# Kernel optimization log

Hardware: AMD Instinct MI355X
Metric: run time of the kernel (lower is better)

The kernel has to match this reference:

```python
import jax, jax.numpy as jnp
import numpy as np

EMB = 1024
HEADS = 16

def setup_inputs() -> dict:
    key = jax.random.key(0)
    ks = jax.random.split(key, 9)
    s = 1.0 / np.sqrt(EMB)
    x = jax.random.normal(ks[0], (2, 2048, EMB), dtype=jnp.float32)
    Wq = jax.random.normal(ks[1], (EMB, EMB), dtype=jnp.float32) * s
    bq = jax.random.normal(ks[2], (EMB,), dtype=jnp.float32) * s
    Wk = jax.random.normal(ks[3], (EMB, EMB), dtype=jnp.float32) * s
    bk = jax.random.normal(ks[4], (EMB,), dtype=jnp.float32) * s
    Wv = jax.random.normal(ks[5], (EMB, EMB), dtype=jnp.float32) * s
    bv = jax.random.normal(ks[6], (EMB,), dtype=jnp.float32) * s
    Wo = jax.random.normal(ks[7], (EMB, EMB), dtype=jnp.float32) * s
    bo = jax.random.normal(ks[8], (EMB,), dtype=jnp.float32) * s
    return {"x": x, "Wq": Wq, "bq": bq, "Wk": Wk, "bk": bk, "Wv": Wv, "bv": bv, "Wo": Wo, "bo": bo}

def reference(x, Wq, bq, Wk, bk, Wv, bv, Wo, bo):
    B, N, E = x.shape
    H = HEADS
    D = E // H
    # q/k/v projections, split heads: b n (h d) -> b h n d
    def proj(W, b):
        y = jnp.einsum('bne,ef->bnf', x, W.T) + b
        return y.reshape(B, N, H, D).transpose(0, 2, 1, 3)
    q = proj(Wq, bq)
    k = proj(Wk, bk)
    v = proj(Wv, bv)
    energy = jnp.einsum('bhqd,bhkd->bhqk', q, k)
    scaling = jnp.asarray(E, x.dtype) ** 0.5  # note: sqrt(emb_size), as in source
    att = jax.nn.softmax(energy / scaling, axis=-1)
    out = jnp.einsum('bhqk,bhkd->bhqd', att, v)
    out = out.transpose(0, 2, 1, 3).reshape(B, N, E)  # b h n d -> b n (h d)
    return jnp.einsum('bne,ef->bnf', out, Wo.T) + bo
```

## Files before the change

### kernel.cpp

```cpp
#include <hip/hip_runtime.h>
#include <hip/hip_bf16.h>
#include <stdint.h>

typedef __bf16 bf16;
typedef __bf16 bf16x8 __attribute__((ext_vector_type(8)));
typedef __bf16 bf16x4 __attribute__((ext_vector_type(4)));
typedef __bf16 bf16x2 __attribute__((ext_vector_type(2)));
typedef float  f32x4  __attribute__((ext_vector_type(4)));
typedef float  f32x16 __attribute__((ext_vector_type(16)));
typedef unsigned int uint;

#define MFMA(a,b,c)   __builtin_amdgcn_mfma_f32_16x16x32_bf16((a),(b),(c),0,0,0)
#define MFMA32(a,b,c) __builtin_amdgcn_mfma_f32_32x32x16_bf16((a),(b),(c),0,0,0)
#define EXP2(x)       __builtin_amdgcn_exp2f(x)

__device__ __forceinline__ void gload_lds16(const void* g, void* lds) {
  __builtin_amdgcn_global_load_lds(
      (const __attribute__((address_space(1))) uint32_t*)g,
      (__attribute__((address_space(3))) uint32_t*)lds, 16, 0, 0);
}

__device__ __forceinline__ uint pk_bf16(float lo, float hi) {
  bf16x2 v; v[0] = (bf16)lo; v[1] = (bf16)hi;
  return __builtin_bit_cast(uint, v);
}

__global__ __launch_bounds__(256) void k_cvt(
    const float* __restrict__ x,
    const float* __restrict__ wq, const float* __restrict__ wk,
    const float* __restrict__ wv, const float* __restrict__ wo,
    bf16* __restrict__ xb, bf16* __restrict__ wqb, bf16* __restrict__ wkb,
    bf16* __restrict__ wvb, bf16* __restrict__ wob)
{
  int r = blockIdx.y;
  const float* s; bf16* d; int n;
  switch (r) {
    case 0: s = x;  d = xb;  n = 4194304; break;
    case 1: s = wq; d = wqb; n = 1048576; break;
    case 2: s = wk; d = wkb; n = 1048576; break;
    case 3: s = wv; d = wvb; n = 1048576; break;
    default: s = wo; d = wob; n = 1048576; break;
  }
  int i = (blockIdx.x * 256 + threadIdx.x) * 8;
  if (i >= n) return;
  const float4* sp = (const float4*)(s + i);
  float4 a = sp[0], b = sp[1];
  bf16x8 o;
  o[0]=(bf16)a.x; o[1]=(bf16)a.y; o[2]=(bf16)a.z; o[3]=(bf16)a.w;
  o[4]=(bf16)b.x; o[5]=(bf16)b.y; o[6]=(bf16)b.z; o[7]=(bf16)b.w;
  *(bf16x8*)(d + i) = o;
}

__global__ __launch_bounds__(256) void k_gemm_qkv(
    const bf16* __restrict__ A,
    const bf16* __restrict__ Wq, const bf16* __restrict__ Wk, const bf16* __restrict__ Wv,
    const float* __restrict__ bq, const float* __restrict__ bk, const float* __restrict__ bv,
    bf16* __restrict__ Qw, bf16* __restrict__ Kw, bf16* __restrict__ Vtw)
{
  __shared__ __align__(16) char As[8192];
  __shared__ __align__(16) char Bs[8192];
  int tid = threadIdx.x;
  int wv4 = tid >> 6, l = tid & 63, lo = l & 15, hi = l >> 4;
  int mt = blockIdx.x;
  int ft = blockIdx.y;
  int wsel = ft >> 3;
  const bf16* W = (wsel == 0) ? Wq : (wsel == 1) ? Wk : Wv;
  const float* bias = (wsel == 0) ? bq : (wsel == 1) ? bk : bv;
  int f0 = (ft & 7) * 128;
  const bf16* Ab = A + (size_t)mt * 128 * 1024;
  const bf16* Wb = W + (size_t)f0 * 1024;
  int wm = wv4 >> 1, wf = wv4 & 1;
  f32x4 acc[4][4];
  #pragma unroll
  for (int i = 0; i < 4; i++)
    #pragma unroll
    for (int j = 0; j < 4; j++) acc[i][j] = (f32x4){0.f, 0.f, 0.f, 0.f};

  for (int k0 = 0; k0 < 1024; k0 += 32) {
    __syncthreads();
    #pragma unroll
    for (int p = 0; p < 2; p++) {
      int e = p * 256 + tid;
      int row = e >> 2, sl = e & 3;
      gload_lds16(Ab + row * 1024 + k0 + sl * 8, As + (p * 256 + wv4 * 64) * 16);
      gload_lds16(Wb + row * 1024 + k0 + sl * 8, Bs + (p * 256 + wv4 * 64) * 16);
    }
    __syncthreads();
    bf16x8 af[4], bfr[4];
    #pragma unroll
    for (int ms = 0; ms < 4; ms++)
      af[ms] = *(const bf16x8*)(As + ((wm * 64 + ms * 16 + lo) * 32 + hi * 8) * 2);
    #pragma unroll
    for (int fs = 0; fs < 4; fs++)
      bfr[fs] = *(const bf16x8*)(Bs + ((wf * 64 + fs * 16 + lo) * 32 + hi * 8) * 2);
    #pragma unroll
    for (int ms = 0; ms < 4; ms++)
      #pragma unroll
      for (int fs = 0; fs < 4; fs++)
        acc[ms][fs] = MFMA(af[ms], bfr[fs], acc[ms][fs]);
  }

  float bv4[4];
  #pragma unroll
  for (int fs = 0; fs < 4; fs++) bv4[fs] = bias[f0 + wf * 64 + fs * 16 + lo];
  #pragma unroll
  for (int ms = 0; ms < 4; ms++) {
    #pragma unroll
    for (int fs = 0; fs < 4; fs++) {
      int fl = f0 + wf * 64 + fs * 16 + lo;
      int h = fl >> 6, dd = fl & 63;
      #pragma unroll
      for (int r = 0; r < 4; r++) {
        int m = mt * 128 + wm * 64 + ms * 16 + hi * 4 + r;
        int b = m >> 11, n = m & 2047;
        float val = acc[ms][fs][r] + bv4[fs];
        if (wsel == 0)      Qw[(((size_t)(b * 16 + h) * 2048 + n) * 64) + dd] = (bf16)(val * 0.0450842199527801f);
        else if (wsel == 1) Kw[(((size_t)(b * 16 + h) * 2048 + n) * 64) + dd] = (bf16)val;
        else                Vtw[(((size_t)(b * 16 + h) * 64 + dd) * 2048) + n] = (bf16)val;
      }
    }
  }
}

__global__ __launch_bounds__(256, 1) void k_attn(
    const bf16* __restrict__ Q, const bf16* __restrict__ K,
    const bf16* __restrict__ Vt, bf16* __restrict__ O)
{
  __shared__ __align__(16) char Ks[2][8192];
  __shared__ __align__(16) char Vs[2][8192];
  int tid = threadIdx.x;
  int wid = tid >> 6, l = tid & 63;
  int lq = l & 31, hi1 = l >> 5;
  int qt = blockIdx.x, bh = blockIdx.y;
  int q0 = qt * 256 + wid * 64;
  const bf16* Kb = K + (size_t)bh * 2048 * 64;
  const bf16* Vb = Vt + (size_t)bh * 64 * 2048;
  const bf16* Qb = Q + ((size_t)bh * 2048 + q0) * 64 + hi1 * 8;

  bf16x8 qf0[4], qf1[4];
  #pragma unroll
  for (int c = 0; c < 4; c++) {
    qf0[c] = *(const bf16x8*)(Qb + (size_t)lq * 64 + 16 * c);
    qf1[c] = *(const bf16x8*)(Qb + (size_t)(lq + 32) * 64 + 16 * c);
  }

  f32x16 o00, o01, o10, o11;
  f32x16 zz;
  #pragma unroll
  for (int r = 0; r < 16; r++) { zz[r] = 0.f; o00[r] = 0.f; o01[r] = 0.f; o10[r] = 0.f; o11[r] = 0.f; }
  float ls0 = 0.f, ls1 = 0.f;

  int srow = tid >> 3, slot = tid & 7;
  int swz = 16 * (slot ^ (srow & 7));
  int swk = lq & 7;
  uint4 k0r, k1r, v0r, v1r;
  #define STAGE(t) {                                                          \
    k0r = *(const uint4*)(Kb + (size_t)((t)*64 + srow) * 64 + slot * 8);      \
    k1r = *(const uint4*)(Kb + (size_t)((t)*64 + srow + 32) * 64 + slot * 8); \
    v0r = *(const uint4*)(Vb + (size_t)srow * 2048 + (t)*64 + slot * 8);      \
    v1r = *(const uint4*)(Vb + (size_t)(srow + 32) * 2048 + (t)*64 + slot * 8); }
  #define WRBUF(bi) {                                  \
    *(uint4*)(Ks[bi] + srow * 128 + swz)        = k0r; \
    *(uint4*)(Ks[bi] + (srow + 32) * 128 + swz) = k1r; \
    *(uint4*)(Vs[bi] + srow * 128 + swz)        = v0r; \
    *(uint4*)(Vs[bi] + (srow + 32) * 128 + swz) = v1r; }
  #define EXPSUM(S, T0, T1, T2, T3)                     \
    _Pragma("unroll")                                   \
    for (int r = 0; r < 16; r += 4) {                   \
      S[r]   = EXP2(S[r]);   T0 += S[r];                \
      S[r+1] = EXP2(S[r+1]); T1 += S[r+1];              \
      S[r+2] = EXP2(S[r+2]); T2 += S[r+2];              \
      S[r+3] = EXP2(S[r+3]); T3 += S[r+3];              \
    }
  #define PACK(dst, plo, phi)                                                \
    _Pragma("unroll")                                                        \
    for (int m = 0; m < 2; m++) {                                            \
      uint a0 = pk_bf16(plo[8*m+0], plo[8*m+1]);                             \
      uint b0 = pk_bf16(plo[8*m+4], plo[8*m+5]);                             \
      asm volatile("v_permlane32_swap_b32 %0, %1" : "+v"(a0), "+v"(b0));     \
      uint a1 = pk_bf16(plo[8*m+2], plo[8*m+3]);                             \
      uint b1 = pk_bf16(plo[8*m+6], plo[8*m+7]);                             \
      asm volatile("v_permlane32_swap_b32 %0, %1" : "+v"(a1), "+v"(b1));     \
      dst[m] = (uint4){a0, a1, b0, b1};                                      \
      uint c0 = pk_bf16(phi[8*m+0], phi[8*m+1]);                             \
      uint d0 = pk_bf16(phi[8*m+4], phi[8*m+5]);                             \
      asm volatile("v_permlane32_swap_b32 %0, %1" : "+v"(c0), "+v"(d0));     \
      uint c1 = pk_bf16(phi[8*m+2], phi[8*m+3]);                             \
      uint d1 = pk_bf16(phi[8*m+6], phi[8*m+7]);                             \
      asm volatile("v_permlane32_swap_b32 %0, %1" : "+v"(c1), "+v"(d1));     \
      dst[2+m] = (uint4){c0, c1, d0, d1};                                    \
    }

  STAGE(0);
  WRBUF(0);
  STAGE(1);

  for (int t = 0; t < 32; ++t) {
    __syncthreads();
    const char* Kc = Ks[t & 1];
    const char* Vc = Vs[t & 1];

    bf16x8 kf0[4], kf1[4];
    #pragma unroll
    for (int c = 0; c < 4; c++) {
      kf0[c] = *(const bf16x8*)(Kc + lq * 128 + 16 * ((2*c + hi1) ^ swk));
      kf1[c] = *(const bf16x8*)(Kc + (32 + lq) * 128 + 16 * ((2*c + hi1) ^ swk));
    }

    __builtin_amdgcn_s_setprio(1);
    f32x16 s00 = MFMA32(kf0[0], qf0[0], zz);
    f32x16 s01 = MFMA32(kf1[0], qf0[0], zz);
    f32x16 s10 = MFMA32(kf0[0], qf1[0], zz);
    f32x16 s11 = MFMA32(kf1[0], qf1[0], zz);
    #pragma unroll
    for (int c = 1; c < 4; c++) {
      s00 = MFMA32(kf0[c], qf0[c], s00);
      s01 = MFMA32(kf1[c], qf0[c], s01);
      s10 = MFMA32(kf0[c], qf1[c], s10);
      s11 = MFMA32(kf1[c], qf1[c], s11);
    }
    __builtin_amdgcn_s_setprio(0);

    float t0 = 0.f, t1 = 0.f, t2 = 0.f, t3 = 0.f;
    float u0 = 0.f, u1 = 0.f, u2 = 0.f, u3 = 0.f;
    EXPSUM(s00, t0, t1, t2, t3);
    EXPSUM(s01, t0, t1, t2, t3);
    EXPSUM(s10, u0, u1, u2, u3);
    EXPSUM(s11, u0, u1, u2, u3);
    ls0 += (t0 + t1) + (t2 + t3);
    ls1 += (u0 + u1) + (u2 + u3);

    uint4 pf0[4], pf1[4];
    PACK(pf0, s00, s01);
    PACK(pf1, s10, s11);

    __builtin_amdgcn_s_setprio(1);
    #pragma unroll
    for (int c = 0; c < 4; c++) {
      bf16x8 vf0 = *(const bf16x8*)(Vc + lq * 128 + 16 * ((2*c + hi1) ^ swk));
      bf16x8 vf1 = *(const bf16x8*)(Vc + (32 + lq) * 128 + 16 * ((2*c + hi1) ^ swk));
      bf16x8 p0b = __builtin_bit_cast(bf16x8, pf0[c]);
      bf16x8 p1b = __builtin_bit_cast(bf16x8, pf1[c]);
      o00 = MFMA32(vf0, p0b, o00);
      o01 = MFMA32(vf1, p0b, o01);
      o10 = MFMA32(vf0, p1b, o10);
      o11 = MFMA32(vf1, p1b, o11);
    }
    __builtin_amdgcn_s_setprio(0);

    if (t < 31) {
      WRBUF((t + 1) & 1);
      if (t < 30) STAGE(t + 2);
    }
  }
  #undef STAGE
  #undef WRBUF

  float l0 = ls0 + __shfl_xor(ls0, 32);
  float l1 = ls1 + __shfl_xor(ls1, 32);
  float inv0 = 1.0f / l0, inv1 = 1.0f / l1;
  int b = bh >> 4, h = bh & 15;
  bf16* Ob0 = O + ((size_t)(b * 2048 + q0 + lq)) * 1024 + h * 64 + hi1 * 4;
  bf16* Ob1 = O + ((size_t)(b * 2048 + q0 + 32 + lq)) * 1024 + h * 64 + hi1 * 4;
  #pragma unroll
  for (int g = 0; g < 4; g++) {
    bf16x4 w0, w1, w2, w3;
    #pragma unroll
    for (int j = 0; j < 4; j++) {
      w0[j] = (bf16)(o00[4*g+j] * inv0);
      w1[j] = (bf16)(o01[4*g+j] * inv0);
      w2[j] = (bf16)(o10[4*g+j] * inv1);
      w3[j] = (bf16)(o11[4*g+j] * inv1);
    }
    *(bf16x4*)(Ob0 + g * 8)      = w0;
    *(bf16x4*)(Ob0 + 32 + g * 8) = w1;
    *(bf16x4*)(Ob1 + g * 8)      = w2;
    *(bf16x4*)(Ob1 + 32 + g * 8) = w3;
  }
}

__global__ __launch_bounds__(256) void k_gemm_out(
    const bf16* __restrict__ A,
    const bf16* __restrict__ W,
    const float* __restrict__ bias,
    float* __restrict__ Cout)
{
  __shared__ __align__(16) char As[8192];
  __shared__ __align__(16) char Bs[8192];
  int tid = threadIdx.x;
  int wv4 = tid >> 6, l = tid & 63, lo = l & 15, hi = l >> 4;
  int mt = blockIdx.x;
  int f0 = blockIdx.y * 128;
  const bf16* Ab = A + (size_t)mt * 128 * 1024;
  const bf16* Wb = W + (size_t)f0 * 1024;
  int wm = wv4 >> 1, wf = wv4 & 1;
  f32x4 acc[4][4];
  #pragma unroll
  for (int i = 0; i < 4; i++)
    #pragma unroll
    for (int j = 0; j < 4; j++) acc[i][j] = (f32x4){0.f, 0.f, 0.f, 0.f};

  for (int k0 = 0; k0 < 1024; k0 += 32) {
    __syncthreads();
    #pragma unroll
    for (int p = 0; p < 2; p++) {
      int e = p * 256 + tid;
      int row = e >> 2, sl = e & 3;
      gload_lds16(Ab + row * 1024 + k0 + sl * 8, As + (p * 256 + wv4 * 64) * 16);
      gload_lds16(Wb + row * 1024 + k0 + sl * 8, Bs + (p * 256 + wv4 * 64) * 16);
    }
    __syncthreads();
    bf16x8 af[4], bfr[4];
    #pragma unroll
    for (int ms = 0; ms < 4; ms++)
      af[ms] = *(const bf16x8*)(As + ((wm * 64 + ms * 16 + lo) * 32 + hi * 8) * 2);
    #pragma unroll
    for (int fs = 0; fs < 4; fs++)
      bfr[fs] = *(const bf16x8*)(Bs + ((wf * 64 + fs * 16 + lo) * 32 + hi * 8) * 2);
    #pragma unroll
    for (int ms = 0; ms < 4; ms++)
      #pragma unroll
      for (int fs = 0; fs < 4; fs++)
        acc[ms][fs] = MFMA(af[ms], bfr[fs], acc[ms][fs]);
  }

  float bv4[4];
  #pragma unroll
  for (int fs = 0; fs < 4; fs++) bv4[fs] = bias[f0 + wf * 64 + fs * 16 + lo];
  #pragma unroll
  for (int ms = 0; ms < 4; ms++)
    #pragma unroll
    for (int fs = 0; fs < 4; fs++) {
      int f = f0 + wf * 64 + fs * 16 + lo;
      #pragma unroll
      for (int r = 0; r < 4; r++) {
        int m = mt * 128 + wm * 64 + ms * 16 + hi * 4 + r;
        Cout[(size_t)m * 1024 + f] = acc[ms][fs][r] + bv4[fs];
      }
    }
}

extern "C" void kernel_launch(void* const* d_in, const int* in_sizes, int n_in,
                              void* d_out, int out_size, void* d_ws, size_t ws_size,
                              hipStream_t stream) {
  const float* x  = (const float*)d_in[0];
  const float* Wq = (const float*)d_in[1];
  const float* bq = (const float*)d_in[2];
  const float* Wk = (const float*)d_in[3];
  const float* bk = (const float*)d_in[4];
  const float* Wv = (const float*)d_in[5];
  const float* bv = (const float*)d_in[6];
  const float* Wo = (const float*)d_in[7];
  const float* bo = (const float*)d_in[8];
  float* out = (float*)d_out;
  char* ws = (char*)d_ws;

  bf16* xb  = (bf16*)(ws);
  bf16* wqb = (bf16*)(ws + 8388608);
  bf16* wkb = (bf16*)(ws + 10485760);
  bf16* wvb = (bf16*)(ws + 12582912);
  bf16* wob = (bf16*)(ws + 14680064);
  bf16* Qw  = (bf16*)(ws + 16777216);
  bf16* Kw  = (bf16*)(ws + 25165824);
  bf16* Vtw = (bf16*)(ws + 33554432);
  bf16* Ow  = (bf16*)(ws + 41943040);

  k_cvt<<<dim3(2048, 5), 256, 0, stream>>>(x, Wq, Wk, Wv, Wo, xb, wqb, wkb, wvb, wob);
  k_gemm_qkv<<<dim3(32, 24), 256, 0, stream>>>(xb, wqb, wkb, wvb, bq, bk, bv, Qw, Kw, Vtw);
  k_attn<<<dim3(8, 32), 256, 0, stream>>>(Qw, Kw, Vtw, Ow);
  k_gemm_out<<<dim3(32, 8), 256, 0, stream>>>(Ow, wob, bo, out);
}
```

Before: 126.1 us.

## Halve attention per-wave query tile to 32 rows and double grid

Each wave in the attention kernel now handles 32 query rows instead of 64, so a block covers 128 queries and the grid doubles to 16x32 blocks. Launch bounds are raised to allow two blocks per CU, cutting accumulator and Q-fragment registers so more waves can hide latency. The cost is that each K/V tile staged in LDS is reused across half as many queries, doubling K/V global loads and LDS traffic per unit of work.

```diff
diff --git a/kernel.cpp b/kernel.cpp
--- a/kernel.cpp
+++ b/kernel.cpp
@@ -122,7 +122,7 @@
   }
 }
 
-__global__ __launch_bounds__(256, 1) void k_attn(
+__global__ __launch_bounds__(256, 2) void k_attn(
     const bf16* __restrict__ Q, const bf16* __restrict__ K,
     const bf16* __restrict__ Vt, bf16* __restrict__ O)
 {
@@ -132,23 +132,19 @@
   int wid = tid >> 6, l = tid & 63;
   int lq = l & 31, hi1 = l >> 5;
   int qt = blockIdx.x, bh = blockIdx.y;
-  int q0 = qt * 256 + wid * 64;
+  int qg = qt * 128 + wid * 32 + lq;
   const bf16* Kb = K + (size_t)bh * 2048 * 64;
   const bf16* Vb = Vt + (size_t)bh * 64 * 2048;
-  const bf16* Qb = Q + ((size_t)bh * 2048 + q0) * 64 + hi1 * 8;
-
-  bf16x8 qf0[4], qf1[4];
-  #pragma unroll
-  for (int c = 0; c < 4; c++) {
-    qf0[c] = *(const bf16x8*)(Qb + (size_t)lq * 64 + 16 * c);
-    qf1[c] = *(const bf16x8*)(Qb + (size_t)(lq + 32) * 64 + 16 * c);
-  }
-
-  f32x16 o00, o01, o10, o11;
-  f32x16 zz;
-  #pragma unroll
-  for (int r = 0; r < 16; r++) { zz[r] = 0.f; o00[r] = 0.f; o01[r] = 0.f; o10[r] = 0.f; o11[r] = 0.f; }
-  float ls0 = 0.f, ls1 = 0.f;
+
+  bf16x8 qf[4];
+  const bf16* Qb = Q + ((size_t)bh * 2048 + qg) * 64 + hi1 * 8;
+  #pragma unroll
+  for (int c = 0; c < 4; c++) qf[c] = *(const bf16x8*)(Qb + 16 * c);
+
+  f32x16 o0, o1, zz;
+  #pragma unroll
+  for (int r = 0; r < 16; r++) { zz[r] = 0.f; o0[r] = 0.f; o1[r] = 0.f; }
+  float ls = 0.f;
 
   int srow = tid >> 3, slot = tid & 7;
   int swz = 16 * (slot ^ (srow & 7));
@@ -208,43 +204,31 @@
     }
 
     __builtin_amdgcn_s_setprio(1);
-    f32x16 s00 = MFMA32(kf0[0], qf0[0], zz);
-    f32x16 s01 = MFMA32(kf1[0], qf0[0], zz);
-    f32x16 s10 = MFMA32(kf0[0], qf1[0], zz);
-    f32x16 s11 = MFMA32(kf1[0], qf1[0], zz);
+    f32x16 s0 = MFMA32(kf0[0], qf[0], zz);
+    f32x16 s1 = MFMA32(kf1[0], qf[0], zz);
     #pragma unroll
     for (int c = 1; c < 4; c++) {
-      s00 = MFMA32(kf0[c], qf0[c], s00);
-      s01 = MFMA32(kf1[c], qf0[c], s01);
-      s10 = MFMA32(kf0[c], qf1[c], s10);
-      s11 = MFMA32(kf1[c], qf1[c], s11);
+      s0 = MFMA32(kf0[c], qf[c], s0);
+      s1 = MFMA32(kf1[c], qf[c], s1);
     }
     __builtin_amdgcn_s_setprio(0);
 
     float t0 = 0.f, t1 = 0.f, t2 = 0.f, t3 = 0.f;
-    float u0 = 0.f, u1 = 0.f, u2 = 0.f, u3 = 0.f;
-    EXPSUM(s00, t0, t1, t2, t3);
-    EXPSUM(s01, t0, t1, t2, t3);
-    EXPSUM(s10, u0, u1, u2, u3);
-    EXPSUM(s11, u0, u1, u2, u3);
-    ls0 += (t0 + t1) + (t2 + t3);
-    ls1 += (u0 + u1) + (u2 + u3);
-
-    uint4 pf0[4], pf1[4];
-    PACK(pf0, s00, s01);
-    PACK(pf1, s10, s11);
+    EXPSUM(s0, t0, t1, t2, t3);
+    EXPSUM(s1, t0, t1, t2, t3);
+    ls += (t0 + t1) + (t2 + t3);
+
+    uint4 pf[4];
+    PACK(pf, s0, s1);
 
     __builtin_amdgcn_s_setprio(1);
     #pragma unroll
     for (int c = 0; c < 4; c++) {
+      bf16x8 pb = __builtin_bit_cast(bf16x8, pf[c]);
       bf16x8 vf0 = *(const bf16x8*)(Vc + lq * 128 + 16 * ((2*c + hi1) ^ swk));
+      o0 = MFMA32(vf0, pb, o0);
       bf16x8 vf1 = *(const bf16x8*)(Vc + (32 + lq) * 128 + 16 * ((2*c + hi1) ^ swk));
-      bf16x8 p0b = __builtin_bit_cast(bf16x8, pf0[c]);
-      bf16x8 p1b = __builtin_bit_cast(bf16x8, pf1[c]);
-      o00 = MFMA32(vf0, p0b, o00);
-      o01 = MFMA32(vf1, p0b, o01);
-      o10 = MFMA32(vf0, p1b, o10);
-      o11 = MFMA32(vf1, p1b, o11);
+      o1 = MFMA32(vf1, pb, o1);
     }
     __builtin_amdgcn_s_setprio(0);
 
@@ -256,26 +240,20 @@
   #undef STAGE
   #undef WRBUF
 
-  float l0 = ls0 + __shfl_xor(ls0, 32);
-  float l1 = ls1 + __shfl_xor(ls1, 32);
-  float inv0 = 1.0f / l0, inv1 = 1.0f / l1;
+  float lsum = ls + __shfl_xor(ls, 32);
+  float inv = 1.0f / lsum;
   int b = bh >> 4, h = bh & 15;
-  bf16* Ob0 = O + ((size_t)(b * 2048 + q0 + lq)) * 1024 + h * 64 + hi1 * 4;
-  bf16* Ob1 = O + ((size_t)(b * 2048 + q0 + 32 + lq)) * 1024 + h * 64 + hi1 * 4;
+  bf16* Ob = O + ((size_t)(b * 2048 + qg)) * 1024 + h * 64 + hi1 * 4;
   #pragma unroll
   for (int g = 0; g < 4; g++) {
-    bf16x4 w0, w1, w2, w3;
+    bf16x4 w0, w1;
     #pragma unroll
     for (int j = 0; j < 4; j++) {
-      w0[j] = (bf16)(o00[4*g+j] * inv0);
-      w1[j] = (bf16)(o01[4*g+j] * inv0);
-      w2[j] = (bf16)(o10[4*g+j] * inv1);
-      w3[j] = (bf16)(o11[4*g+j] * inv1);
-    }
-    *(bf16x4*)(Ob0 + g * 8)      = w0;
-    *(bf16x4*)(Ob0 + 32 + g * 8) = w1;
-    *(bf16x4*)(Ob1 + g * 8)      = w2;
-    *(bf16x4*)(Ob1 + 32 + g * 8) = w3;
+      w0[j] = (bf16)(o0[4*g+j] * inv);
+      w1[j] = (bf16)(o1[4*g+j] * inv);
+    }
+    *(bf16x4*)(Ob + g * 8)      = w0;
+    *(bf16x4*)(Ob + 32 + g * 8) = w1;
   }
 }
 
@@ -367,6 +345,6 @@
 
   k_cvt<<<dim3(2048, 5), 256, 0, stream>>>(x, Wq, Wk, Wv, Wo, xb, wqb, wkb, wvb, wob);
   k_gemm_qkv<<<dim3(32, 24), 256, 0, stream>>>(xb, wqb, wkb, wvb, bq, bk, bv, Qw, Kw, Vtw);
-  k_attn<<<dim3(8, 32), 256, 0, stream>>>(Qw, Kw, Vtw, Ow);
+  k_attn<<<dim3(16, 32), 256, 0, stream>>>(Qw, Kw, Vtw, Ow);
   k_gemm_out<<<dim3(32, 8), 256, 0, stream>>>(Ow, wob, bo, out);
 }
```

After: 116.6 us. 7.5% less time.
